# Performance work log

Hardware: AMD Instinct MI355X
Metric: run time of the kernel (lower is better)

The kernel has to match this reference:

```python
import jax, jax.numpy as jnp
import numpy as np


def setup_inputs() -> dict:
    key = jax.random.key(0)
    ks = jax.random.split(key, 10)
    B, S, V, E, C = 256, 512, 50000, 300, 10
    sentences = jax.random.randint(ks[0], (B, S), 0, V)
    emb_table = jax.random.normal(ks[1], (V, E), dtype=jnp.float32) * 0.1
    # pad_token=0 row zeroed like nn.Embedding(padding_idx=0)
    emb_table = emb_table.at[0].set(0.0)
    k3 = jax.random.normal(ks[2], (3, E), dtype=jnp.float32) * 0.05
    b3 = jax.random.normal(ks[3], (1,), dtype=jnp.float32) * 0.05
    k4 = jax.random.normal(ks[4], (4, E), dtype=jnp.float32) * 0.05
    b4 = jax.random.normal(ks[5], (1,), dtype=jnp.float32) * 0.05
    k5 = jax.random.normal(ks[6], (5, E), dtype=jnp.float32) * 0.05
    b5 = jax.random.normal(ks[7], (1,), dtype=jnp.float32) * 0.05
    fc_w = jax.random.normal(ks[8], (C, 3), dtype=jnp.float32) * 0.1
    fc_b = jax.random.normal(ks[9], (C,), dtype=jnp.float32) * 0.1
    return {"sentences": sentences, "emb_table": emb_table,
            "k3": k3, "b3": b3, "k4": k4, "b4": b4, "k5": k5, "b5": b5,
            "fc_w": fc_w, "fc_b": fc_b}


def _window_feature(emb, k, b):
    # emb: [B,S,E]; k: [w,E]; conv with 1 in/1 out channel spanning full E (VALID)
    out = jax.lax.conv_general_dilated(
        emb[:, None, :, :],            # [B,1,S,E]
        k[None, None, :, :],           # [1,1,w,E]
        window_strides=(1, 1), padding="VALID")  # [B,1,S-w+1,1]
    f = jnp.tanh(out[:, 0, :, 0] + b)  # [B,S-w+1]
    return f.max(axis=-1)              # [B]


def reference(sentences, emb_table, k3, b3, k4, b4, k5, b5, fc_w, fc_b):
    emb = emb_table[sentences]  # [B,S,E]
    feats = jnp.stack([_window_feature(emb, k3, b3),
                       _window_feature(emb, k4, b4),
                       _window_feature(emb, k5, b5)], axis=-1)  # [B,3]
    # dropout is identity in eval mode
    logits = feats @ fc_w.T + fc_b  # [B,C]
    return jax.nn.log_softmax(logits, axis=-1)
```

## Files before the change

kernel.cpp:

```cpp
#include <hip/hip_runtime.h>
#include <hip/hip_bf16.h>
#include <math.h>

#define NSENT 256
#define SLEN  512
#define VROWS 50000
#define EDIM  300
#define NROW  12
#define NSTEP 10

typedef __attribute__((ext_vector_type(8))) short bf16x8;
typedef __attribute__((ext_vector_type(4))) float f32x4;

static __device__ __forceinline__ short f2bf(float f) {
    __hip_bfloat16 h = __float2bfloat16(f);
    short s;
    __builtin_memcpy(&s, &h, sizeof(s));
    return s;
}

__global__ __launch_bounds__(256, 4)
void vocab_scores_mfma(const float* __restrict__ emb,
                       const float* __restrict__ k3,
                       const float* __restrict__ k4,
                       const float* __restrict__ k5,
                       float* __restrict__ s)
{
    __shared__ bf16x8 bfrag_lds[NSTEP * 64];

    const int tid  = threadIdx.x;
    const int lane = tid & 63;
    const int wave = tid >> 6;
    const int rc   = lane & 15;
    const int kg   = lane >> 4;

    for (int e = tid; e < NSTEP * 64; e += 256) {
        const int st  = e >> 6;
        const int le  = e & 63;
        const int rce = le & 15;
        const int kge = le >> 4;
        const float* krow = nullptr;
        if      (rce < 3)  krow = k3 + rce * EDIM;
        else if (rce < 7)  krow = k4 + (rce - 3) * EDIM;
        else if (rce < 12) krow = k5 + (rce - 7) * EDIM;
        const int k0 = st * 32 + kge * 8;
        float4 b0 = make_float4(0.f,0.f,0.f,0.f);
        float4 b1 = make_float4(0.f,0.f,0.f,0.f);
        if (krow) {
            if (k0 + 4 <= EDIM) b0 = *reinterpret_cast<const float4*>(krow + k0);
            if (k0 + 8 <= EDIM) b1 = *reinterpret_cast<const float4*>(krow + k0 + 4);
        }
        bf16x8 f;
        f[0]=f2bf(b0.x); f[1]=f2bf(b0.y); f[2]=f2bf(b0.z); f[3]=f2bf(b0.w);
        f[4]=f2bf(b1.x); f[5]=f2bf(b1.y); f[6]=f2bf(b1.z); f[7]=f2bf(b1.w);
        bfrag_lds[e] = f;
    }
    __syncthreads();

    const int vbase = blockIdx.x * 64 + wave * 16;
    const int vrow  = min(vbase + rc, VROWS - 1);
    const float* arow = emb + (size_t)vrow * EDIM;

    f32x4 acc = {0.f, 0.f, 0.f, 0.f};

    #pragma unroll
    for (int half = 0; half < 2; ++half) {
        float4 a0[5], a1[5];
        #pragma unroll
        for (int i = 0; i < 5; ++i) {
            const int k0 = (half * 5 + i) * 32 + kg * 8;
            a0[i] = (k0 + 4 <= EDIM)
                  ? *reinterpret_cast<const float4*>(arow + k0)
                  : make_float4(0.f,0.f,0.f,0.f);
            a1[i] = (k0 + 8 <= EDIM)
                  ? *reinterpret_cast<const float4*>(arow + k0 + 4)
                  : make_float4(0.f,0.f,0.f,0.f);
        }
        #pragma unroll
        for (int i = 0; i < 5; ++i) {
            const int st = half * 5 + i;
            const bf16x8 bf = bfrag_lds[st * 64 + lane];
            bf16x8 af;
            af[0]=f2bf(a0[i].x); af[1]=f2bf(a0[i].y);
            af[2]=f2bf(a0[i].z); af[3]=f2bf(a0[i].w);
            af[4]=f2bf(a1[i].x); af[5]=f2bf(a1[i].y);
            af[6]=f2bf(a1[i].z); af[7]=f2bf(a1[i].w);
            acc = __builtin_amdgcn_mfma_f32_16x16x32_bf16(af, bf, acc, 0, 0, 0);
        }
    }

    if (rc < NROW) {
        #pragma unroll
        for (int j = 0; j < 4; ++j) {
            const int v = vbase + kg * 4 + j;
            if (v < VROWS) s[(size_t)v * NROW + rc] = acc[j];
        }
    }
}

__global__ __launch_bounds__(1024, 1)
void textcnn_finish(const int*   __restrict__ sent,
                    const float* __restrict__ s,
                    const float* __restrict__ b3,
                    const float* __restrict__ b4,
                    const float* __restrict__ b5,
                    const float* __restrict__ fcw,
                    const float* __restrict__ fcb,
                    float* __restrict__ out)
{
    __shared__ float s_lds[NROW * SLEN];
    __shared__ float red[8][3];

    const int b = blockIdx.x;
    const int t = threadIdx.x;

    auto gather = [&](int token, int j) {
        const int widx = sent[b * SLEN + token];
        const float4 v = reinterpret_cast<const float4*>(s + (size_t)widx * NROW)[j];
        s_lds[(4*j + 0) * SLEN + token] = v.x;
        s_lds[(4*j + 1) * SLEN + token] = v.y;
        s_lds[(4*j + 2) * SLEN + token] = v.z;
        s_lds[(4*j + 3) * SLEN + token] = v.w;
    };

    gather(t & 511, t >> 9);
    if (t < SLEN) gather(t, 2);
    __syncthreads();

    if (t < SLEN) {
        const float bb3 = b3[0], bb4 = b4[0], bb5 = b5[0];
        float m3 = -1e30f, m4 = -1e30f, m5 = -1e30f;
        if (t < SLEN - 2)
            m3 = tanhf(s_lds[0*SLEN + t] + s_lds[1*SLEN + t+1] +
                       s_lds[2*SLEN + t+2] + bb3);
        if (t < SLEN - 3)
            m4 = tanhf(s_lds[3*SLEN + t] + s_lds[4*SLEN + t+1] +
                       s_lds[5*SLEN + t+2] + s_lds[6*SLEN + t+3] + bb4);
        if (t < SLEN - 4)
            m5 = tanhf(s_lds[7*SLEN + t] + s_lds[8*SLEN + t+1] +
                       s_lds[9*SLEN + t+2] + s_lds[10*SLEN + t+3] +
                       s_lds[11*SLEN + t+4] + bb5);

        #pragma unroll
        for (int off = 32; off; off >>= 1) {
            m3 = fmaxf(m3, __shfl_xor(m3, off));
            m4 = fmaxf(m4, __shfl_xor(m4, off));
            m5 = fmaxf(m5, __shfl_xor(m5, off));
        }
        if ((t & 63) == 0) {
            const int w = t >> 6;
            red[w][0] = m3; red[w][1] = m4; red[w][2] = m5;
        }
    }
    __syncthreads();

    if (t == 0) {
        float f3 = red[0][0], f4 = red[0][1], f5 = red[0][2];
        #pragma unroll
        for (int w = 1; w < 8; ++w) {
            f3 = fmaxf(f3, red[w][0]);
            f4 = fmaxf(f4, red[w][1]);
            f5 = fmaxf(f5, red[w][2]);
        }
        float lg[10];
        float mx = -1e30f;
        #pragma unroll
        for (int c = 0; c < 10; ++c) {
            lg[c] = fcb[c] + f3 * fcw[c*3+0] + f4 * fcw[c*3+1] + f5 * fcw[c*3+2];
            mx = fmaxf(mx, lg[c]);
        }
        float ssum = 0.f;
        #pragma unroll
        for (int c = 0; c < 10; ++c) ssum += expf(lg[c] - mx);
        const float lse = logf(ssum);
        #pragma unroll
        for (int c = 0; c < 10; ++c) out[b * 10 + c] = lg[c] - mx - lse;
    }
}

extern "C" void kernel_launch(void* const* d_in, const int* in_sizes, int n_in,
                              void* d_out, int out_size, void* d_ws, size_t ws_size,
                              hipStream_t stream) {
    const int*   sent = (const int*)  d_in[0];
    const float* emb  = (const float*)d_in[1];
    const float* k3   = (const float*)d_in[2];
    const float* b3   = (const float*)d_in[3];
    const float* k4   = (const float*)d_in[4];
    const float* b4   = (const float*)d_in[5];
    const float* k5   = (const float*)d_in[6];
    const float* b5   = (const float*)d_in[7];
    const float* fcw  = (const float*)d_in[8];
    const float* fcb  = (const float*)d_in[9];
    float* out = (float*)d_out;
    float* s   = (float*)d_ws;

    const int nblk = (VROWS + 63) / 64;
    vocab_scores_mfma<<<nblk, 256, 0, stream>>>(emb, k3, k4, k5, s);
    textcnn_finish<<<NSENT, 1024, 0, stream>>>(sent, s, b3, b4, b5, fcw, fcb, out);
}
```

Measured before the change: 24.57 us.

## Stage embedding tile through LDS with coalesced loads before MFMA

Each block now loads its 64×300 fp32 embedding tile with fully contiguous float4 loads across all threads. It converts the tile to bf16 into a padded LDS buffer, and the MFMA loop then reads its A fragments from LDS. Before, each lane read from per-row strided addresses. The aim is better global-load coalescing and fewer VMEM instructions in this memory-bound pass. In exchange it uses about 40 KB more LDS per block and a large register prefetch array, with launch bounds dropped to 3 blocks per SM. The K-tail reads columns 300–319, which land in uninitialized LDS padding or spill into the next row. Those products are multiplied by zero weights, but they would still give NaN if the padding happens to hold NaN bit patterns.

```diff
diff --git a/kernel.cpp b/kernel.cpp
--- a/kernel.cpp
+++ b/kernel.cpp
@@ -8,8 +8,13 @@
 #define EDIM  300
 #define NROW  12
 #define NSTEP 10
+#define TROWS 64
+#define NF4   75
+#define TF4   (TROWS*NF4)
+#define LSTR  312
 
 typedef __attribute__((ext_vector_type(8))) short bf16x8;
+typedef __attribute__((ext_vector_type(4))) short bf16x4;
 typedef __attribute__((ext_vector_type(4))) float f32x4;
 
 static __device__ __forceinline__ short f2bf(float f) {
@@ -19,13 +24,14 @@
     return s;
 }
 
-__global__ __launch_bounds__(256, 4)
+__global__ __launch_bounds__(256, 3)
 void vocab_scores_mfma(const float* __restrict__ emb,
                        const float* __restrict__ k3,
                        const float* __restrict__ k4,
                        const float* __restrict__ k5,
                        float* __restrict__ s)
 {
+    __shared__ short  ebuf[TROWS * LSTR];
     __shared__ bf16x8 bfrag_lds[NSTEP * 64];
 
     const int tid  = threadIdx.x;
@@ -33,6 +39,21 @@
     const int wave = tid >> 6;
     const int rc   = lane & 15;
     const int kg   = lane >> 4;
+
+    const int vbase = blockIdx.x * TROWS;
+    const float4* embf4 = reinterpret_cast<const float4*>(emb);
+
+    float4 pre[19];
+    #pragma unroll
+    for (int i = 0; i < 19; ++i) {
+        const int g = i * 256 + tid;
+        if (g < TF4) {
+            const int row  = g / NF4;
+            const int col  = g % NF4;
+            const int grow = min(vbase + row, VROWS - 1);
+            pre[i] = embf4[(size_t)grow * NF4 + col];
+        }
+    }
 
     for (int e = tid; e < NSTEP * 64; e += 256) {
         const int st  = e >> 6;
@@ -55,44 +76,35 @@
         f[4]=f2bf(b1.x); f[5]=f2bf(b1.y); f[6]=f2bf(b1.z); f[7]=f2bf(b1.w);
         bfrag_lds[e] = f;
     }
+
+    #pragma unroll
+    for (int i = 0; i < 19; ++i) {
+        const int g = i * 256 + tid;
+        if (g < TF4) {
+            const int row = g / NF4;
+            const int col = g % NF4;
+            bf16x4 w;
+            w[0]=f2bf(pre[i].x); w[1]=f2bf(pre[i].y);
+            w[2]=f2bf(pre[i].z); w[3]=f2bf(pre[i].w);
+            *reinterpret_cast<bf16x4*>(&ebuf[row * LSTR + col * 4]) = w;
+        }
+    }
     __syncthreads();
 
-    const int vbase = blockIdx.x * 64 + wave * 16;
-    const int vrow  = min(vbase + rc, VROWS - 1);
-    const float* arow = emb + (size_t)vrow * EDIM;
-
+    const int r0 = wave * 16 + rc;
     f32x4 acc = {0.f, 0.f, 0.f, 0.f};
-
     #pragma unroll
-    for (int half = 0; half < 2; ++half) {
-        float4 a0[5], a1[5];
-        #pragma unroll
-        for (int i = 0; i < 5; ++i) {
-            const int k0 = (half * 5 + i) * 32 + kg * 8;
-            a0[i] = (k0 + 4 <= EDIM)
-                  ? *reinterpret_cast<const float4*>(arow + k0)
-                  : make_float4(0.f,0.f,0.f,0.f);
-            a1[i] = (k0 + 8 <= EDIM)
-                  ? *reinterpret_cast<const float4*>(arow + k0 + 4)
-                  : make_float4(0.f,0.f,0.f,0.f);
-        }
-        #pragma unroll
-        for (int i = 0; i < 5; ++i) {
-            const int st = half * 5 + i;
-            const bf16x8 bf = bfrag_lds[st * 64 + lane];
-            bf16x8 af;
-            af[0]=f2bf(a0[i].x); af[1]=f2bf(a0[i].y);
-            af[2]=f2bf(a0[i].z); af[3]=f2bf(a0[i].w);
-            af[4]=f2bf(a1[i].x); af[5]=f2bf(a1[i].y);
-            af[6]=f2bf(a1[i].z); af[7]=f2bf(a1[i].w);
-            acc = __builtin_amdgcn_mfma_f32_16x16x32_bf16(af, bf, acc, 0, 0, 0);
-        }
+    for (int st = 0; st < NSTEP; ++st) {
+        const bf16x8 af = *reinterpret_cast<const bf16x8*>(
+                              &ebuf[r0 * LSTR + st * 32 + kg * 8]);
+        const bf16x8 bf = bfrag_lds[st * 64 + lane];
+        acc = __builtin_amdgcn_mfma_f32_16x16x32_bf16(af, bf, acc, 0, 0, 0);
     }
 
     if (rc < NROW) {
         #pragma unroll
         for (int j = 0; j < 4; ++j) {
-            const int v = vbase + kg * 4 + j;
+            const int v = vbase + wave * 16 + kg * 4 + j;
             if (v < VROWS) s[(size_t)v * NROW + rc] = acc[j];
         }
     }
@@ -194,7 +206,7 @@
     float* out = (float*)d_out;
     float* s   = (float*)d_ws;
 
-    const int nblk = (VROWS + 63) / 64;
+    const int nblk = (VROWS + TROWS - 1) / TROWS;
     vocab_scores_mfma<<<nblk, 256, 0, stream>>>(emb, k3, k4, k5, s);
     textcnn_finish<<<NSENT, 1024, 0, stream>>>(sent, s, b3, b4, b5, fcw, fcb, out);
 }
```

After: 27.19 us. +10.6%, slower.

## Fuse vocab scoring and sentence reduction into one kernel with grid barrier

Applied to the files above, without the earlier changes.

Merges the vocabulary-score MFMA kernel and the per-sentence gather/tanh/max/log-softmax kernel into one launch of 256 blocks. Each wave now processes 3–4 row tiles of 16 vocab rows in sequence. Blocks then meet at a software grid barrier built on an atomic counter in the workspace, which is reset by a memset each call, before the per-sentence phase runs. The aim is to remove the second kernel launch and the gap between kernels. In exchange, far fewer waves are in flight to hide the memory latency of streaming the embedding table. Correctness also depends on all 256 blocks being resident at once.

```diff
diff --git a/kernel.cpp b/kernel.cpp
--- a/kernel.cpp
+++ b/kernel.cpp
@@ -8,6 +8,8 @@
 #define EDIM  300
 #define NROW  12
 #define NSTEP 10
+#define NTILE 3125
+#define CNT_OFF (8u << 20)
 
 typedef __attribute__((ext_vector_type(8))) short bf16x8;
 typedef __attribute__((ext_vector_type(4))) float f32x4;
@@ -20,13 +22,19 @@
 }
 
 __global__ __launch_bounds__(256, 4)
-void vocab_scores_mfma(const float* __restrict__ emb,
-                       const float* __restrict__ k3,
-                       const float* __restrict__ k4,
-                       const float* __restrict__ k5,
-                       float* __restrict__ s)
+void textcnn_fused(const int*   __restrict__ sent,
+                   const float* __restrict__ emb,
+                   const float* __restrict__ k3, const float* __restrict__ b3,
+                   const float* __restrict__ k4, const float* __restrict__ b4,
+                   const float* __restrict__ k5, const float* __restrict__ b5,
+                   const float* __restrict__ fcw, const float* __restrict__ fcb,
+                   float* __restrict__ out,
+                   float* __restrict__ s,
+                   unsigned int* __restrict__ cnt)
 {
     __shared__ bf16x8 bfrag_lds[NSTEP * 64];
+    __shared__ float  s_lds[NROW * SLEN];
+    __shared__ float  red[4][3];
 
     const int tid  = threadIdx.x;
     const int lane = tid & 63;
@@ -57,124 +65,129 @@
     }
     __syncthreads();
 
-    const int vbase = blockIdx.x * 64 + wave * 16;
-    const int vrow  = min(vbase + rc, VROWS - 1);
-    const float* arow = emb + (size_t)vrow * EDIM;
-
-    f32x4 acc = {0.f, 0.f, 0.f, 0.f};
-
-    #pragma unroll
-    for (int half = 0; half < 2; ++half) {
-        float4 a0[5], a1[5];
+    const int gw = blockIdx.x * 4 + wave;
+    int t0, nt;
+    if (gw < 53) { t0 = gw * 4;      nt = 4; }
+    else         { t0 = gw * 3 + 53; nt = 3; }
+    for (int it = 0; it < nt; ++it) {
+        const int vbase = (t0 + it) * 16;
+        const float* arow = emb + (size_t)(vbase + rc) * EDIM;
+        f32x4 acc = {0.f, 0.f, 0.f, 0.f};
         #pragma unroll
-        for (int i = 0; i < 5; ++i) {
-            const int k0 = (half * 5 + i) * 32 + kg * 8;
-            a0[i] = (k0 + 4 <= EDIM)
-                  ? *reinterpret_cast<const float4*>(arow + k0)
-                  : make_float4(0.f,0.f,0.f,0.f);
-            a1[i] = (k0 + 8 <= EDIM)
-                  ? *reinterpret_cast<const float4*>(arow + k0 + 4)
-                  : make_float4(0.f,0.f,0.f,0.f);
-        }
+        for (int half = 0; half < 2; ++half) {
+            float4 a0[5], a1[5];
+            #pragma unroll
+            for (int i = 0; i < 5; ++i) {
+                const int k0 = (half * 5 + i) * 32 + kg * 8;
+                a0[i] = (k0 + 4 <= EDIM)
+                      ? *reinterpret_cast<const float4*>(arow + k0)
+                      : make_float4(0.f,0.f,0.f,0.f);
+                a1[i] = (k0 + 8 <= EDIM)
+                      ? *reinterpret_cast<const float4*>(arow + k0 + 4)
+                      : make_float4(0.f,0.f,0.f,0.f);
+            }
+            #pragma unroll
+            for (int i = 0; i < 5; ++i) {
+                const int st = half * 5 + i;
+                const bf16x8 bf = bfrag_lds[st * 64 + lane];
+                bf16x8 af;
+                af[0]=f2bf(a0[i].x); af[1]=f2bf(a0[i].y);
+                af[2]=f2bf(a0[i].z); af[3]=f2bf(a0[i].w);
+                af[4]=f2bf(a1[i].x); af[5]=f2bf(a1[i].y);
+                af[6]=f2bf(a1[i].z); af[7]=f2bf(a1[i].w);
+                acc = __builtin_amdgcn_mfma_f32_16x16x32_bf16(af, bf, acc, 0,0,0);
+            }
+        }
+        if (rc < NROW) {
+            #pragma unroll
+            for (int j = 0; j < 4; ++j)
+                s[(size_t)(vbase + kg * 4 + j) * NROW + rc] = acc[j];
+        }
+    }
+
+    const int b  = blockIdx.x;
+    const int w0 = sent[b * SLEN + tid];
+    const int w1 = sent[b * SLEN + 256 + tid];
+    const float bb3 = b3[0], bb4 = b4[0], bb5 = b5[0];
+
+    __syncthreads();
+    if (tid == 0) {
+        __hip_atomic_fetch_add(cnt, 1u, __ATOMIC_RELEASE,
+                               __HIP_MEMORY_SCOPE_AGENT);
+        while (__hip_atomic_load(cnt, __ATOMIC_ACQUIRE,
+                                 __HIP_MEMORY_SCOPE_AGENT) < (unsigned)NSENT)
+            __builtin_amdgcn_s_sleep(2);
+    }
+    __syncthreads();
+
+    {
+        const float4* r0p = reinterpret_cast<const float4*>(s + (size_t)w0 * NROW);
+        const float4* r1p = reinterpret_cast<const float4*>(s + (size_t)w1 * NROW);
+        const float4 sa0 = r0p[0], sb0 = r0p[1], sc0 = r0p[2];
+        const float4 sa1 = r1p[0], sb1 = r1p[1], sc1 = r1p[2];
+
+        const int ta = tid, tb = tid + 256;
+        s_lds[ 0*SLEN+ta]=sa0.x; s_lds[ 1*SLEN+ta]=sa0.y;
+        s_lds[ 2*SLEN+ta]=sa0.z; s_lds[ 3*SLEN+ta]=sa0.w;
+        s_lds[ 4*SLEN+ta]=sb0.x; s_lds[ 5*SLEN+ta]=sb0.y;
+        s_lds[ 6*SLEN+ta]=sb0.z; s_lds[ 7*SLEN+ta]=sb0.w;
+        s_lds[ 8*SLEN+ta]=sc0.x; s_lds[ 9*SLEN+ta]=sc0.y;
+        s_lds[10*SLEN+ta]=sc0.z; s_lds[11*SLEN+ta]=sc0.w;
+        s_lds[ 0*SLEN+tb]=sa1.x; s_lds[ 1*SLEN+tb]=sa1.y;
+        s_lds[ 2*SLEN+tb]=sa1.z; s_lds[ 3*SLEN+tb]=sa1.w;
+        s_lds[ 4*SLEN+tb]=sb1.x; s_lds[ 5*SLEN+tb]=sb1.y;
+        s_lds[ 6*SLEN+tb]=sb1.z; s_lds[ 7*SLEN+tb]=sb1.w;
+        s_lds[ 8*SLEN+tb]=sc1.x; s_lds[ 9*SLEN+tb]=sc1.y;
+        s_lds[10*SLEN+tb]=sc1.z; s_lds[11*SLEN+tb]=sc1.w;
+        __syncthreads();
+
+        float m3 = -1e30f, m4 = -1e30f, m5 = -1e30f;
         #pragma unroll
-        for (int i = 0; i < 5; ++i) {
-            const int st = half * 5 + i;
-            const bf16x8 bf = bfrag_lds[st * 64 + lane];
-            bf16x8 af;
-            af[0]=f2bf(a0[i].x); af[1]=f2bf(a0[i].y);
-            af[2]=f2bf(a0[i].z); af[3]=f2bf(a0[i].w);
-            af[4]=f2bf(a1[i].x); af[5]=f2bf(a1[i].y);
-            af[6]=f2bf(a1[i].z); af[7]=f2bf(a1[i].w);
-            acc = __builtin_amdgcn_mfma_f32_16x16x32_bf16(af, bf, acc, 0, 0, 0);
-        }
-    }
-
-    if (rc < NROW) {
-        #pragma unroll
-        for (int j = 0; j < 4; ++j) {
-            const int v = vbase + kg * 4 + j;
-            if (v < VROWS) s[(size_t)v * NROW + rc] = acc[j];
-        }
-    }
-}
-
-__global__ __launch_bounds__(1024, 1)
-void textcnn_finish(const int*   __restrict__ sent,
-                    const float* __restrict__ s,
-                    const float* __restrict__ b3,
-                    const float* __restrict__ b4,
-                    const float* __restrict__ b5,
-                    const float* __restrict__ fcw,
-                    const float* __restrict__ fcb,
-                    float* __restrict__ out)
-{
-    __shared__ float s_lds[NROW * SLEN];
-    __shared__ float red[8][3];
-
-    const int b = blockIdx.x;
-    const int t = threadIdx.x;
-
-    auto gather = [&](int token, int j) {
-        const int widx = sent[b * SLEN + token];
-        const float4 v = reinterpret_cast<const float4*>(s + (size_t)widx * NROW)[j];
-        s_lds[(4*j + 0) * SLEN + token] = v.x;
-        s_lds[(4*j + 1) * SLEN + token] = v.y;
-        s_lds[(4*j + 2) * SLEN + token] = v.z;
-        s_lds[(4*j + 3) * SLEN + token] = v.w;
-    };
-
-    gather(t & 511, t >> 9);
-    if (t < SLEN) gather(t, 2);
-    __syncthreads();
-
-    if (t < SLEN) {
-        const float bb3 = b3[0], bb4 = b4[0], bb5 = b5[0];
-        float m3 = -1e30f, m4 = -1e30f, m5 = -1e30f;
-        if (t < SLEN - 2)
-            m3 = tanhf(s_lds[0*SLEN + t] + s_lds[1*SLEN + t+1] +
-                       s_lds[2*SLEN + t+2] + bb3);
-        if (t < SLEN - 3)
-            m4 = tanhf(s_lds[3*SLEN + t] + s_lds[4*SLEN + t+1] +
-                       s_lds[5*SLEN + t+2] + s_lds[6*SLEN + t+3] + bb4);
-        if (t < SLEN - 4)
-            m5 = tanhf(s_lds[7*SLEN + t] + s_lds[8*SLEN + t+1] +
-                       s_lds[9*SLEN + t+2] + s_lds[10*SLEN + t+3] +
-                       s_lds[11*SLEN + t+4] + bb5);
-
+        for (int p = 0; p < 2; ++p) {
+            const int t = tid + p * 256;
+            if (t < SLEN - 2)
+                m3 = fmaxf(m3, tanhf(s_lds[0*SLEN + t] + s_lds[1*SLEN + t+1] +
+                                     s_lds[2*SLEN + t+2] + bb3));
+            if (t < SLEN - 3)
+                m4 = fmaxf(m4, tanhf(s_lds[3*SLEN + t] + s_lds[4*SLEN + t+1] +
+                                     s_lds[5*SLEN + t+2] + s_lds[6*SLEN + t+3] + bb4));
+            if (t < SLEN - 4)
+                m5 = fmaxf(m5, tanhf(s_lds[7*SLEN + t] + s_lds[8*SLEN + t+1] +
+                                     s_lds[9*SLEN + t+2] + s_lds[10*SLEN + t+3] +
+                                     s_lds[11*SLEN + t+4] + bb5));
+        }
         #pragma unroll
         for (int off = 32; off; off >>= 1) {
             m3 = fmaxf(m3, __shfl_xor(m3, off));
             m4 = fmaxf(m4, __shfl_xor(m4, off));
             m5 = fmaxf(m5, __shfl_xor(m5, off));
         }
-        if ((t & 63) == 0) {
-            const int w = t >> 6;
-            red[w][0] = m3; red[w][1] = m4; red[w][2] = m5;
-        }
-    }
-    __syncthreads();
-
-    if (t == 0) {
-        float f3 = red[0][0], f4 = red[0][1], f5 = red[0][2];
-        #pragma unroll
-        for (int w = 1; w < 8; ++w) {
-            f3 = fmaxf(f3, red[w][0]);
-            f4 = fmaxf(f4, red[w][1]);
-            f5 = fmaxf(f5, red[w][2]);
-        }
-        float lg[10];
-        float mx = -1e30f;
-        #pragma unroll
-        for (int c = 0; c < 10; ++c) {
-            lg[c] = fcb[c] + f3 * fcw[c*3+0] + f4 * fcw[c*3+1] + f5 * fcw[c*3+2];
-            mx = fmaxf(mx, lg[c]);
-        }
-        float ssum = 0.f;
-        #pragma unroll
-        for (int c = 0; c < 10; ++c) ssum += expf(lg[c] - mx);
-        const float lse = logf(ssum);
-        #pragma unroll
-        for (int c = 0; c < 10; ++c) out[b * 10 + c] = lg[c] - mx - lse;
+        if (lane == 0) { red[wave][0]=m3; red[wave][1]=m4; red[wave][2]=m5; }
+        __syncthreads();
+
+        if (tid == 0) {
+            float f3 = red[0][0], f4 = red[0][1], f5 = red[0][2];
+            #pragma unroll
+            for (int w = 1; w < 4; ++w) {
+                f3 = fmaxf(f3, red[w][0]);
+                f4 = fmaxf(f4, red[w][1]);
+                f5 = fmaxf(f5, red[w][2]);
+            }
+            float lg[10];
+            float mx = -1e30f;
+            #pragma unroll
+            for (int c = 0; c < 10; ++c) {
+                lg[c] = fcb[c] + f3 * fcw[c*3+0] + f4 * fcw[c*3+1]
+                               + f5 * fcw[c*3+2];
+                mx = fmaxf(mx, lg[c]);
+            }
+            float ssum = 0.f;
+            #pragma unroll
+            for (int c = 0; c < 10; ++c) ssum += expf(lg[c] - mx);
+            const float lse = logf(ssum);
+            #pragma unroll
+            for (int c = 0; c < 10; ++c) out[b * 10 + c] = lg[c] - mx - lse;
+        }
     }
 }
 
@@ -193,8 +206,9 @@
     const float* fcb  = (const float*)d_in[9];
     float* out = (float*)d_out;
     float* s   = (float*)d_ws;
-
-    const int nblk = (VROWS + 63) / 64;
-    vocab_scores_mfma<<<nblk, 256, 0, stream>>>(emb, k3, k4, k5, s);
-    textcnn_finish<<<NSENT, 1024, 0, stream>>>(sent, s, b3, b4, b5, fcw, fcb, out);
+    unsigned int* cnt = (unsigned int*)((char*)d_ws + CNT_OFF);
+
+    hipMemsetAsync(cnt, 0, 64, stream);
+    textcnn_fused<<<NSENT, 256, 0, stream>>>(sent, emb, k3, b3, k4, b4,
+                                             k5, b5, fcw, fcb, out, s, cnt);
 }
```

Result: slower. 48.63 us (+97.9%).
